# Optimization experiments

Hardware: AMD Instinct MI355X
Metric: run time of the kernel (lower is better)

The kernel has to match this reference:

```python
import jax, jax.numpy as jnp
import numpy as np

GRID_SIZE = 8
MARGIN = 1.0
NUM_NEG = 8
SOS_NEG = 8
LOSS_LAMBDA = 1.0
D_INTER = 4  # d1_inter_num == d2_inter_num == 4 in the source
IMG = 512    # image side in pixels (H * grid_size)


def warp_points(pts, homo):
    ph = jnp.concatenate([pts, jnp.ones_like(pts[..., :1])], axis=-1)  # B,N,3
    q = jnp.einsum('bij,bnj->bni', homo, ph)
    return q[..., :2] / (q[..., 2:3] + 1e-8)


def inv_sim_vec(d1, d2):
    # 2 - 2*<d1,d2> == squared L2 distance for unit-norm descriptors
    return 2.0 - 2.0 * jnp.sum(d1 * d2, axis=-1)


def inv_sim_mat(d1, d2):
    return 2.0 - 2.0 * jnp.einsum('bnc,bmc->bnm', d1, d2)


def sq_dist_mat(p1, p2):
    # squared Euclidean distance; monotone in distance so topk indices and
    # radius comparisons (vs radius**2) match the original exactly.
    n1 = jnp.sum(p1 * p1, axis=-1)
    n2 = jnp.sum(p2 * p2, axis=-1)
    d = n1[:, :, None] + n2[:, None, :] - 2.0 * jnp.einsum('bnd,bmd->bnm', p1, p2)
    return jnp.maximum(d, 0.0)


def topk_smallest(x, k):
    v, i = jax.lax.top_k(-x, k)
    return -v, i


def create_coo_grid(h, w, grid_size):
    ys, xs = jnp.meshgrid(jnp.arange(h, dtype=jnp.float32), jnp.arange(w, dtype=jnp.float32), indexing='ij')
    return jnp.stack([(xs + 0.5) * grid_size, (ys + 0.5) * grid_size], axis=-1).reshape(-1, 2)  # HW,2 (x,y)


def sample_descriptors(desc, kp, grid_size):
    # desc: B,C,H,W; kp: B,N,2 (x,y) image coords. Bilinear sample + L2 normalize.
    b, c, h, w = desc.shape
    x = kp[..., 0] / grid_size - 0.5
    y = kp[..., 1] / grid_size - 0.5
    x0 = jnp.floor(x); y0 = jnp.floor(y)
    wx = x - x0; wy = y - y0
    x0i = jnp.clip(x0.astype(jnp.int32), 0, w - 1); x1i = jnp.clip(x0i + 1, 0, w - 1)
    y0i = jnp.clip(y0.astype(jnp.int32), 0, h - 1); y1i = jnp.clip(y0i + 1, 0, h - 1)
    dflat = desc.transpose(0, 2, 3, 1).reshape(b, h * w, c)  # B,HW,C
    bi = jnp.arange(b)[:, None]
    g = lambda yi, xi: dflat[bi, yi * w + xi]  # B,N,C
    out = ((1 - wx) * (1 - wy))[..., None] * g(y0i, x0i) \
        + (wx * (1 - wy))[..., None] * g(y0i, x1i) \
        + ((1 - wx) * wy)[..., None] * g(y1i, x0i) \
        + (wx * wy)[..., None] * g(y1i, x1i)
    return out / (jnp.linalg.norm(out, axis=-1, keepdims=True) + 1e-8)


def setup_inputs():
    key = jax.random.key(0)
    k1, k2, k3, k4 = jax.random.split(key, 4)
    b, n, c, h, w = 4, 1024, 128, 64, 64
    kp1 = jax.random.uniform(k1, (b, n, 2), dtype=jnp.float32) * (IMG - 1.0)
    kp1_desc = jax.random.normal(k2, (b, n, c), dtype=jnp.float32)
    kp1_desc = kp1_desc / jnp.linalg.norm(kp1_desc, axis=-1, keepdims=True)
    desc2 = jax.random.normal(k3, (b, c, h, w), dtype=jnp.float32)
    homo12 = jnp.broadcast_to(jnp.eye(3, dtype=jnp.float32), (b, 3, 3)) + 0.005 * jax.random.normal(k4, (b, 3, 3), dtype=jnp.float32)
    w_kp1 = jnp.clip(warp_points(kp1, homo12), 0.0, IMG - 1.0)
    return {'kp1': kp1, 'w_kp1': w_kp1, 'kp1_desc': kp1_desc, 'desc2': desc2, 'homo12': homo12}


def reference(kp1, w_kp1, kp1_desc, desc2, homo12):
    b, n, c = kp1_desc.shape
    _, _, h, w = desc2.shape
    hw = h * w
    gs = GRID_SIZE
    bi = jnp.arange(b)[:, None]

    w_kp1_desc = sample_descriptors(desc2, w_kp1, gs)                 # B,N,C
    positive_sim = inv_sim_vec(kp1_desc, w_kp1_desc)                  # B,N

    coo = jnp.broadcast_to(create_coo_grid(h, w, gs), (b, hw, 2))     # B,HW,2
    # 4 nearest grid cells of each kp1, warped into image 2
    _, kp1_cell_ids = topk_smallest(sq_dist_mat(kp1, coo), D_INTER)   # B,N,4
    kp1_cells = coo[bi, kp1_cell_ids.reshape(b, -1)]                  # B,4N,2
    w_kp1_cells = warp_points(kp1_cells, homo12)                      # B,4N,2
    _, kp2_cell_ids = topk_smallest(sq_dist_mat(w_kp1_cells, coo), D_INTER)  # B,4N,4
    mask = jnp.zeros((b, n * D_INTER, hw), dtype=jnp.float32)
    mask = mask.at[jnp.arange(b)[:, None, None], jnp.arange(n * D_INTER)[None, :, None], kp2_cell_ids].set(1.0)
    neigh_mask = mask.reshape(b, n, D_INTER, hw).sum(axis=2)          # B,N,HW

    desc2_flat = desc2.transpose(0, 2, 3, 1).reshape(b, hw, c)
    desc_sim = inv_sim_mat(kp1_desc, desc2_flat) + neigh_mask * 5.0   # B,N,HW
    neg_sim, _ = topk_smallest(desc_sim, NUM_NEG)                     # B,N,num_neg
    fos = jnp.mean(jnp.maximum(positive_sim[:, :, None] - neg_sim + MARGIN, 0.0) ** 2)

    radius2 = (gs * np.sqrt(2.0) + 0.1) ** 2
    kp1_sim = inv_sim_mat(kp1_desc, kp1_desc) + (sq_dist_mat(kp1, kp1) <= radius2).astype(jnp.float32) * 5.0
    w_kp1_sim = inv_sim_mat(w_kp1_desc, w_kp1_desc) + (sq_dist_mat(w_kp1, w_kp1) <= radius2).astype(jnp.float32) * 5.0
    _, kp1_neg_ids = topk_smallest(kp1_sim, SOS_NEG)                  # B,N,sos_neg
    _, w_kp1_neg_ids = topk_smallest(w_kp1_sim, SOS_NEG)
    b3 = jnp.arange(b)[:, None, None]
    kp1_neg_desc = kp1_desc[b3, kp1_neg_ids]                          # B,N,sos_neg,C
    w_kp1_neg_desc = w_kp1_desc[b3, w_kp1_neg_ids]
    sos = inv_sim_vec(kp1_desc[:, :, None, :], kp1_neg_desc) - inv_sim_vec(w_kp1_desc[:, :, None, :], w_kp1_neg_desc)
    sos = jnp.mean(jnp.sqrt(jnp.sum(sos ** 2, axis=-1)))
    return (fos + sos) * LOSS_LAMBDA
```

## Files before the change

kernel.cpp:

```cpp
#include <hip/hip_runtime.h>

#define NB 4
#define NN 1024
#define NCCH 128
#define NH 64
#define NW 64
#define NHW 4096

constexpr float RADIUS2 = 130.27274173013714f;

typedef __attribute__((ext_vector_type(8))) short short8v;
typedef __attribute__((ext_vector_type(4))) float f32x4;

__device__ __forceinline__ unsigned short f2bf(float f) {
    unsigned u = __float_as_uint(f);
    unsigned r = u + 0x7FFFu + ((u >> 16) & 1u);
    return (unsigned short)(r >> 16);
}
__device__ __forceinline__ float bf2f(unsigned short h) {
    return __uint_as_float(((unsigned)h) << 16);
}

__device__ __forceinline__ void bsort8(float* v) {
    #pragma unroll
    for (int d = 4; d >= 1; d >>= 1) {
        #pragma unroll
        for (int i = 0; i < 8; ++i) {
            if ((i & d) == 0) {
                float x = v[i], y = v[i + d];
                v[i] = fminf(x, y);
                v[i + d] = fmaxf(x, y);
            }
        }
    }
}
__device__ __forceinline__ void merge8(const float* a, const float* b, float* o) {
    #pragma unroll
    for (int k = 0; k < 8; ++k) o[k] = fminf(a[k], b[7 - k]);
    bsort8(o);
}

__device__ __forceinline__ void nearest4(float x, float y, int out_ids[4]) {
    float u = x * 0.125f - 0.5f;
    float v = y * 0.125f - 0.5f;
    u = fminf(fmaxf(u, -1e6f), 1e6f);
    v = fminf(fmaxf(v, -1e6f), 1e6f);
    int iu = (int)floorf(u);
    int iv = (int)floorf(v);
    int xlo = min(max(iu - 2, 0), 60);
    int xhi = max(min(iu + 3, 63), 3);
    int ylo = min(max(iv - 2, 0), 60);
    int yhi = max(min(iv + 3, 63), 3);
    float bd0 = 1e30f, bd1 = 1e30f, bd2 = 1e30f, bd3 = 1e30f;
    int bi0 = 0, bi1 = 0, bi2 = 0, bi3 = 0;
    for (int yy = ylo; yy <= yhi; ++yy) {
        float dy = y - ((float)yy + 0.5f) * 8.0f;
        float dy2 = dy * dy;
        for (int xx = xlo; xx <= xhi; ++xx) {
            float dx = x - ((float)xx + 0.5f) * 8.0f;
            float d = dx * dx + dy2;
            int id = (yy << 6) | xx;
            if (d < bd3) {
                if (d < bd2) {
                    bd3 = bd2; bi3 = bi2;
                    if (d < bd1) {
                        bd2 = bd1; bi2 = bi1;
                        if (d < bd0) { bd1 = bd0; bi1 = bi0; bd0 = d; bi0 = id; }
                        else         { bd1 = d;  bi1 = id; }
                    } else { bd2 = d; bi2 = id; }
                } else { bd3 = d; bi3 = id; }
            }
        }
    }
    out_ids[0] = bi0; out_ids[1] = bi1; out_ids[2] = bi2; out_ids[3] = bi3;
}

__global__ __launch_bounds__(256) void d2split_kernel(
    const float* __restrict__ desc2,
    unsigned short* __restrict__ d2hi, unsigned short* __restrict__ d2lo,
    float* __restrict__ d2T, int use_t)
{
    __shared__ float sT[64][33];
    int bid = blockIdx.x;
    int b = bid >> 8;
    int rem = bid & 255;
    int hw0 = (rem >> 2) * 64;
    int c0 = (rem & 3) * 32;
    int t = threadIdx.x;

    {
        int lane = t & 63, cg = t >> 6;
        const float* src = desc2 + (size_t)b * NCCH * NHW + hw0 + lane;
        #pragma unroll
        for (int i = 0; i < 8; ++i) {
            int cl = cg * 8 + i;
            sT[lane][cl] = src[(size_t)(c0 + cl) * NHW];
        }
    }
    __syncthreads();
    {
        int hw = t >> 2, q = t & 3;
        size_t base = ((size_t)b * NHW + hw0 + hw) * NCCH + c0 + q * 8;
        unsigned short hb[8], lb[8];
        float fb[8];
        #pragma unroll
        for (int i = 0; i < 8; ++i) {
            float f = sT[hw][q * 8 + i];
            unsigned short h = f2bf(f);
            hb[i] = h;
            lb[i] = f2bf(f - bf2f(h));
            fb[i] = f;
        }
        *(short8v*)(d2hi + base) = *(short8v*)hb;
        *(short8v*)(d2lo + base) = *(short8v*)lb;
        if (use_t) {
            *(float4*)(d2T + base) = *(float4*)&fb[0];
            *(float4*)(d2T + base + 4) = *(float4*)&fb[4];
        }
    }
}

__global__ __launch_bounds__(256) void sample_mask_kernel(
    const float* __restrict__ kp1, const float* __restrict__ w_kp1,
    const float* __restrict__ kp1_desc, const float* __restrict__ desc2,
    const float* __restrict__ d2T, int use_t,
    const float* __restrict__ homo,
    unsigned short* __restrict__ khi, unsigned short* __restrict__ klo,
    unsigned short* __restrict__ whi, unsigned short* __restrict__ wlo,
    float* __restrict__ pos_sim, int* __restrict__ mask_ids)
{
    int bid = blockIdx.x;
    if (bid >= 1024) {
        int g = (bid - 1024) * 256 + threadIdx.x;
        if (g >= NB * NN) return;
        int b = g >> 10;
        float x = kp1[g * 2], y = kp1[g * 2 + 1];
        const float* H = homo + b * 9;
        int c4[4];
        nearest4(x, y, c4);
        int out[16];
        #pragma unroll
        for (int k = 0; k < 4; ++k) {
            int id = c4[k];
            float cx = ((float)(id & 63) + 0.5f) * 8.0f;
            float cy = ((float)(id >> 6) + 0.5f) * 8.0f;
            float q0 = H[0] * cx + H[1] * cy + H[2];
            float q1 = H[3] * cx + H[4] * cy + H[5];
            float q2 = H[6] * cx + H[7] * cy + H[8];
            float iz = 1.0f / (q2 + 1e-8f);
            nearest4(q0 * iz, q1 * iz, out + 4 * k);
        }
        #pragma unroll
        for (int k = 0; k < 16; ++k) mask_ids[(size_t)g * 16 + k] = out[k];
        return;
    }

    int lane = threadIdx.x & 63;
    int wid = bid * 4 + (threadIdx.x >> 6);
    int b = wid >> 10;

    float px = w_kp1[wid * 2 + 0], py = w_kp1[wid * 2 + 1];
    float fx = px * 0.125f - 0.5f, fy = py * 0.125f - 0.5f;
    float fx0 = floorf(fx), fy0 = floorf(fy);
    float wx = fx - fx0, wy = fy - fy0;
    int x0 = min(max((int)fx0, 0), NW - 1);
    int x1 = min(x0 + 1, NW - 1);
    int y0 = min(max((int)fy0, 0), NH - 1);
    int y1 = min(y0 + 1, NH - 1);
    float w00 = (1.f - wx) * (1.f - wy), w01 = wx * (1.f - wy);
    float w10 = (1.f - wx) * wy,         w11 = wx * wy;
    int i00 = y0 * NW + x0, i01 = y0 * NW + x1;
    int i10 = y1 * NW + x0, i11 = y1 * NW + x1;

    float o0, o1;
    if (use_t) {
        const float* base = d2T + (size_t)b * NHW * NCCH;
        const float* r00 = base + (size_t)i00 * NCCH;
        const float* r01 = base + (size_t)i01 * NCCH;
        const float* r10 = base + (size_t)i10 * NCCH;
        const float* r11 = base + (size_t)i11 * NCCH;
        o0 = w00 * r00[lane] + w01 * r01[lane] + w10 * r10[lane] + w11 * r11[lane];
        o1 = w00 * r00[lane + 64] + w01 * r01[lane + 64]
           + w10 * r10[lane + 64] + w11 * r11[lane + 64];
    } else {
        const float* d2 = desc2 + (size_t)b * NCCH * NHW;
        const float* p0 = d2 + (size_t)lane * NHW;
        const float* p1 = d2 + (size_t)(lane + 64) * NHW;
        o0 = w00 * p0[i00] + w01 * p0[i01] + w10 * p0[i10] + w11 * p0[i11];
        o1 = w00 * p1[i00] + w01 * p1[i01] + w10 * p1[i10] + w11 * p1[i11];
    }
    float nrm = o0 * o0 + o1 * o1;
    #pragma unroll
    for (int off = 32; off > 0; off >>= 1) nrm += __shfl_xor(nrm, off, 64);
    float inv = 1.0f / (sqrtf(nrm) + 1e-8f);
    o0 *= inv; o1 *= inv;

    float a0 = kp1_desc[(size_t)wid * NCCH + lane];
    float a1 = kp1_desc[(size_t)wid * NCCH + lane + 64];
    float dot = a0 * o0 + a1 * o1;
    #pragma unroll
    for (int off = 32; off > 0; off >>= 1) dot += __shfl_xor(dot, off, 64);

    size_t base = (size_t)wid * NCCH;
    unsigned short h;
    h = f2bf(a0); khi[base + lane] = h;      klo[base + lane] = f2bf(a0 - bf2f(h));
    h = f2bf(a1); khi[base + lane + 64] = h; klo[base + lane + 64] = f2bf(a1 - bf2f(h));
    h = f2bf(o0); whi[base + lane] = h;      wlo[base + lane] = f2bf(o0 - bf2f(h));
    h = f2bf(o1); whi[base + lane + 64] = h; wlo[base + lane + 64] = f2bf(o1 - bf2f(h));
    if (lane == 0) pos_sim[wid] = 2.0f - 2.0f * dot;
}

__global__ __launch_bounds__(256, 4) void simtop_fused(
    const unsigned short* __restrict__ khi, const unsigned short* __restrict__ klo,
    const unsigned short* __restrict__ whi, const unsigned short* __restrict__ wlo,
    const unsigned short* __restrict__ d2hi, const unsigned short* __restrict__ d2lo,
    const float* __restrict__ kp1, const float* __restrict__ w_kp1,
    const int* __restrict__ mask_ids,
    float* __restrict__ fosP, float* __restrict__ sosAP, float* __restrict__ sosBP)
{
    __shared__ float sChunk[32][257];
    __shared__ int   sMask[32][16];
    __shared__ float sCx[256], sCy[256];
    __shared__ float sRx[32], sRy[32];

    int tid = threadIdx.x;
    int bid = blockIdx.x;

    int mode, cs, rg, b, nchunk, colbase, outStride;
    const unsigned short *AH, *AL, *BH, *BL;
    const float* coords = nullptr;
    float* outP;
    if (bid < 512) {
        mode = 0; b = bid >> 7; int rem = bid & 127;
        cs = rem & 3; rg = rem >> 2;
        nchunk = 4; colbase = cs * 1024;
        AH = khi + (size_t)b * NN * NCCH;  AL = klo + (size_t)b * NN * NCCH;
        BH = d2hi + (size_t)b * NHW * NCCH; BL = d2lo + (size_t)b * NHW * NCCH;
        outP = fosP; outStride = 32;
    } else if (bid < 768) {
        int id = bid - 512;
        mode = 1; b = id >> 6; int rem = id & 63;
        cs = rem & 1; rg = rem >> 1;
        nchunk = 2; colbase = cs * 512;
        AH = khi + (size_t)b * NN * NCCH;  AL = klo + (size_t)b * NN * NCCH;
        BH = AH; BL = AL;
        coords = kp1; outP = sosAP; outStride = 16;
    } else {
        int id = bid - 768;
        mode = 2; b = id >> 6; int rem = id & 63;
        cs = rem & 1; rg = rem >> 1;
        nchunk = 2; colbase = cs * 512;
        AH = whi + (size_t)b * NN * NCCH;  AL = wlo + (size_t)b * NN * NCCH;
        BH = AH; BL = AL;
        coords = w_kp1; outP = sosBP; outStride = 16;
    }
    int row0 = rg * 32;

    int lane = tid & 63, wg = tid >> 6;
    int lrow = lane & 15, lgrp = lane >> 4;
    int srow = tid & 31, sgrp = tid >> 5;

    short8v ahi[2][4], alo[2][4];
    #pragma unroll
    for (int rt = 0; rt < 2; ++rt) {
        const unsigned short* aH = AH + (size_t)(row0 + rt * 16 + lrow) * NCCH + lgrp * 8;
        const unsigned short* aL = AL + (size_t)(row0 + rt * 16 + lrow) * NCCH + lgrp * 8;
        #pragma unroll
        for (int s = 0; s < 4; ++s) {
            ahi[rt][s] = *(const short8v*)(aH + s * 32);
            alo[rt][s] = *(const short8v*)(aL + s * 32);
        }
    }

    if (mode == 0) {
        for (int e = tid; e < 512; e += 256)
            sMask[e >> 4][e & 15] =
                mask_ids[((size_t)b * NN + row0 + (e >> 4)) * 16 + (e & 15)];
    } else if (tid < 32) {
        sRx[tid] = coords[((size_t)b * NN + row0 + tid) * 2];
        sRy[tid] = coords[((size_t)b * NN + row0 + tid) * 2 + 1];
    }

    float loc[8];
    #pragma unroll
    for (int k = 0; k < 8; ++k) loc[k] = 1e30f;

    for (int ch = 0; ch < nchunk; ++ch) {
        int cglob = colbase + ch * 256;
        __syncthreads();

        int colq = cglob + wg * 64;
        #pragma unroll
        for (int np = 0; np < 2; ++np) {
            const unsigned short* b0H = BH + (size_t)(colq + (np * 2 + 0) * 16 + lrow) * NCCH + lgrp * 8;
            const unsigned short* b0L = BL + (size_t)(colq + (np * 2 + 0) * 16 + lrow) * NCCH + lgrp * 8;
            const unsigned short* b1H = BH + (size_t)(colq + (np * 2 + 1) * 16 + lrow) * NCCH + lgrp * 8;
            const unsigned short* b1L = BL + (size_t)(colq + (np * 2 + 1) * 16 + lrow) * NCCH + lgrp * 8;
            f32x4 a00 = {0.f, 0.f, 0.f, 0.f}, a01 = {0.f, 0.f, 0.f, 0.f};
            f32x4 a10 = {0.f, 0.f, 0.f, 0.f}, a11 = {0.f, 0.f, 0.f, 0.f};
            #pragma unroll
            for (int s = 0; s < 4; ++s) {
                short8v bh0 = *(const short8v*)(b0H + s * 32);
                short8v bl0 = *(const short8v*)(b0L + s * 32);
                short8v bh1 = *(const short8v*)(b1H + s * 32);
                short8v bl1 = *(const short8v*)(b1L + s * 32);
                a00 = __builtin_amdgcn_mfma_f32_16x16x32_bf16(ahi[0][s], bh0, a00, 0, 0, 0);
                a10 = __builtin_amdgcn_mfma_f32_16x16x32_bf16(ahi[1][s], bh0, a10, 0, 0, 0);
                a01 = __builtin_amdgcn_mfma_f32_16x16x32_bf16(ahi[0][s], bh1, a01, 0, 0, 0);
                a11 = __builtin_amdgcn_mfma_f32_16x16x32_bf16(ahi[1][s], bh1, a11, 0, 0, 0);
                a00 = __builtin_amdgcn_mfma_f32_16x16x32_bf16(ahi[0][s], bl0, a00, 0, 0, 0);
                a10 = __builtin_amdgcn_mfma_f32_16x16x32_bf16(ahi[1][s], bl0, a10, 0, 0, 0);
                a01 = __builtin_amdgcn_mfma_f32_16x16x32_bf16(ahi[0][s], bl1, a01, 0, 0, 0);
                a11 = __builtin_amdgcn_mfma_f32_16x16x32_bf16(ahi[1][s], bl1, a11, 0, 0, 0);
                a00 = __builtin_amdgcn_mfma_f32_16x16x32_bf16(alo[0][s], bh0, a00, 0, 0, 0);
                a10 = __builtin_amdgcn_mfma_f32_16x16x32_bf16(alo[1][s], bh0, a10, 0, 0, 0);
                a01 = __builtin_amdgcn_mfma_f32_16x16x32_bf16(alo[0][s], bh1, a01, 0, 0, 0);
                a11 = __builtin_amdgcn_mfma_f32_16x16x32_bf16(alo[1][s], bh1, a11, 0, 0, 0);
            }
            #pragma unroll
            for (int r = 0; r < 4; ++r) {
                sChunk[lgrp * 4 + r][wg * 64 + (np * 2 + 0) * 16 + lrow]      = 2.0f - 2.0f * a00[r];
                sChunk[16 + lgrp * 4 + r][wg * 64 + (np * 2 + 0) * 16 + lrow] = 2.0f - 2.0f * a10[r];
                sChunk[lgrp * 4 + r][wg * 64 + (np * 2 + 1) * 16 + lrow]      = 2.0f - 2.0f * a01[r];
                sChunk[16 + lgrp * 4 + r][wg * 64 + (np * 2 + 1) * 16 + lrow] = 2.0f - 2.0f * a11[r];
            }
        }
        __syncthreads();

        if (mode == 0) {
            for (int e = tid; e < 512; e += 256) {
                int r = e >> 4;
                int id = sMask[r][e & 15] - cglob;
                if (id >= 0 && id < 256) atomicAdd(&sChunk[r][id], 5.0f);
            }
        } else {
            sCx[tid] = coords[((size_t)b * NN + cglob + tid) * 2];
            sCy[tid] = coords[((size_t)b * NN + cglob + tid) * 2 + 1];
        }
        __syncthreads();

        float rx = 0.f, ry = 0.f;
        if (mode != 0) { rx = sRx[srow]; ry = sRy[srow]; }
        #pragma unroll
        for (int j = 0; j < 32; ++j) {
            int cl = sgrp * 32 + j;
            float v = sChunk[srow][cl];
            if (mode != 0) {
                float dx = rx - sCx[cl], dy = ry - sCy[cl];
                if (dx * dx + dy * dy <= RADIUS2) v += 5.0f;
            }
            if (v < loc[7]) {
                loc[7] = v;
                #pragma unroll
                for (int p = 7; p > 0; --p) {
                    if (loc[p - 1] > loc[p]) {
                        float t = loc[p - 1]; loc[p - 1] = loc[p]; loc[p] = t;
                    }
                }
            }
        }
    }

    __syncthreads();
    float* mg = &sChunk[0][0];
    #pragma unroll
    for (int k = 0; k < 8; ++k) mg[srow * 67 + sgrp * 8 + k] = loc[k];
    __syncthreads();
    #pragma unroll
    for (int step = 1; step < 8; step <<= 1) {
        if ((sgrp & (2 * step - 1)) == 0) {
            float a[8], bb[8], o[8];
            #pragma unroll
            for (int k = 0; k < 8; ++k) {
                a[k]  = mg[srow * 67 + sgrp * 8 + k];
                bb[k] = mg[srow * 67 + (sgrp + step) * 8 + k];
            }
            merge8(a, bb, o);
            #pragma unroll
            for (int k = 0; k < 8; ++k) mg[srow * 67 + sgrp * 8 + k] = o[k];
        }
        __syncthreads();
    }
    if (tid < 32) {
        size_t row = (size_t)b * NN + row0 + tid;
        #pragma unroll
        for (int k = 0; k < 8; ++k)
            outP[row * outStride + cs * 8 + k] = mg[tid * 67 + k];
    }
}

__global__ __launch_bounds__(256) void frow_kernel(
    const float* __restrict__ fosP, const float* __restrict__ sosAP,
    const float* __restrict__ sosBP, const float* __restrict__ pos_sim,
    float* __restrict__ frow, float* __restrict__ srow)
{
    int row = blockIdx.x * 256 + threadIdx.x;
    if (row >= NB * NN) return;

    float l0[8], l1[8], l2[8], l3[8], t0[8], t1[8], m[8];
    const float4* fp = (const float4*)(fosP + (size_t)row * 32);
    float4 q;
    q = fp[0]; l0[0]=q.x; l0[1]=q.y; l0[2]=q.z; l0[3]=q.w;
    q = fp[1]; l0[4]=q.x; l0[5]=q.y; l0[6]=q.z; l0[7]=q.w;
    q = fp[2]; l1[0]=q.x; l1[1]=q.y; l1[2]=q.z; l1[3]=q.w;
    q = fp[3]; l1[4]=q.x; l1[5]=q.y; l1[6]=q.z; l1[7]=q.w;
    q = fp[4]; l2[0]=q.x; l2[1]=q.y; l2[2]=q.z; l2[3]=q.w;
    q = fp[5]; l2[4]=q.x; l2[5]=q.y; l2[6]=q.z; l2[7]=q.w;
    q = fp[6]; l3[0]=q.x; l3[1]=q.y; l3[2]=q.z; l3[3]=q.w;
    q = fp[7]; l3[4]=q.x; l3[5]=q.y; l3[6]=q.z; l3[7]=q.w;
    merge8(l0, l1, t0); merge8(l2, l3, t1); merge8(t0, t1, m);

    float p = pos_sim[row], fs = 0.f;
    #pragma unroll
    for (int k = 0; k < 8; ++k) {
        float h = fmaxf(p - m[k] + 1.0f, 0.f);
        fs += h * h;
    }

    const float4* ap = (const float4*)(sosAP + (size_t)row * 16);
    q = ap[0]; l0[0]=q.x; l0[1]=q.y; l0[2]=q.z; l0[3]=q.w;
    q = ap[1]; l0[4]=q.x; l0[5]=q.y; l0[6]=q.z; l0[7]=q.w;
    q = ap[2]; l1[0]=q.x; l1[1]=q.y; l1[2]=q.z; l1[3]=q.w;
    q = ap[3]; l1[4]=q.x; l1[5]=q.y; l1[6]=q.z; l1[7]=q.w;
    merge8(l0, l1, t0);
    const float4* bp = (const float4*)(sosBP + (size_t)row * 16);
    q = bp[0]; l2[0]=q.x; l2[1]=q.y; l2[2]=q.z; l2[3]=q.w;
    q = bp[1]; l2[4]=q.x; l2[5]=q.y; l2[6]=q.z; l2[7]=q.w;
    q = bp[2]; l3[0]=q.x; l3[1]=q.y; l3[2]=q.z; l3[3]=q.w;
    q = bp[3]; l3[4]=q.x; l3[5]=q.y; l3[6]=q.z; l3[7]=q.w;
    merge8(l2, l3, t1);

    float acc = 0.f;
    #pragma unroll
    for (int k = 0; k < 8; ++k) {
        float d = t0[k] - t1[k];
        acc += d * d;
    }
    frow[row] = fs;
    srow[row] = sqrtf(acc);
}

__global__ __launch_bounds__(256) void freduce_kernel(
    const float* __restrict__ frow, const float* __restrict__ srow,
    float* __restrict__ outp)
{
    __shared__ float sf[256], ss[256];
    int t = threadIdx.x;
    float f = 0.f, s = 0.f;
    for (int i = t; i < NB * NN; i += 256) { f += frow[i]; s += srow[i]; }
    sf[t] = f; ss[t] = s;
    __syncthreads();
    for (int o = 128; o > 0; o >>= 1) {
        if (t < o) { sf[t] += sf[t + o]; ss[t] += ss[t + o]; }
        __syncthreads();
    }
    if (t == 0)
        outp[0] = sf[0] / (float)(NB * NN * 8) + ss[0] / (float)(NB * NN);
}

extern "C" void kernel_launch(void* const* d_in, const int* in_sizes, int n_in,
                              void* d_out, int out_size, void* d_ws, size_t ws_size,
                              hipStream_t stream) {
    const float* kp1      = (const float*)d_in[0];
    const float* w_kp1    = (const float*)d_in[1];
    const float* kp1_desc = (const float*)d_in[2];
    const float* desc2    = (const float*)d_in[3];
    const float* homo     = (const float*)d_in[4];
    float* outp = (float*)d_out;

    char* ws = (char*)d_ws;
    size_t o = 0;
    unsigned short* khi  = (unsigned short*)(ws + o); o += (size_t)NB * NN * NCCH * 2;
    unsigned short* klo  = (unsigned short*)(ws + o); o += (size_t)NB * NN * NCCH * 2;
    unsigned short* whi  = (unsigned short*)(ws + o); o += (size_t)NB * NN * NCCH * 2;
    unsigned short* wlo  = (unsigned short*)(ws + o); o += (size_t)NB * NN * NCCH * 2;
    unsigned short* d2hi = (unsigned short*)(ws + o); o += (size_t)NB * NHW * NCCH * 2;
    unsigned short* d2lo = (unsigned short*)(ws + o); o += (size_t)NB * NHW * NCCH * 2;
    float* pos_sim = (float*)(ws + o); o += (size_t)NB * NN * 4;
    float* fosP    = (float*)(ws + o); o += (size_t)NB * NN * 32 * 4;
    float* sosAP   = (float*)(ws + o); o += (size_t)NB * NN * 16 * 4;
    float* sosBP   = (float*)(ws + o); o += (size_t)NB * NN * 16 * 4;
    float* frow    = (float*)(ws + o); o += (size_t)NB * NN * 4;
    float* srow    = (float*)(ws + o); o += (size_t)NB * NN * 4;
    int*   mask_id = (int*)(ws + o);   o += (size_t)NB * NN * 16 * 4;
    float* d2T     = (float*)(ws + o);
    size_t need_t  = o + (size_t)NB * NHW * NCCH * 4;
    int use_t = (ws_size >= need_t) ? 1 : 0;
    if (!use_t) d2T = (float*)ws;

    d2split_kernel<<<NB * 256, 256, 0, stream>>>(desc2, d2hi, d2lo, d2T, use_t);
    sample_mask_kernel<<<1040, 256, 0, stream>>>(kp1, w_kp1, kp1_desc, desc2,
                                                 d2T, use_t, homo,
                                                 khi, klo, whi, wlo,
                                                 pos_sim, mask_id);
    simtop_fused<<<1024, 256, 0, stream>>>(khi, klo, whi, wlo, d2hi, d2lo,
                                           kp1, w_kp1, mask_id,
                                           fosP, sosAP, sosBP);
    frow_kernel<<<16, 256, 0, stream>>>(fosP, sosAP, sosBP, pos_sim, frow, srow);
    freduce_kernel<<<1, 256, 0, stream>>>(frow, srow, outp);
}
```

Measured before the change: 199.7 us.

## Halve column chunk size and remap blocks so each XCD shares operand panels

The column chunk processed per iteration shrinks from 256 to 128, which halves the shared-memory tile and the per-wave MFMA tile, so more chunks run per block. Block indices are also reassigned so that blocks on the same XCD (bid mod 8) work on the same batch and column slice, improving L2 reuse of the B operand across that XCD's blocks. The trade-off is less MFMA work per synchronisation, more barriers per block, and a launch grid that must still total 1024 blocks in the new layout.

```diff
diff --git a/kernel.cpp b/kernel.cpp
--- a/kernel.cpp
+++ b/kernel.cpp
@@ -6,6 +6,7 @@
 #define NH 64
 #define NW 64
 #define NHW 4096
+#define CHUNK 128
 
 constexpr float RADIUS2 = 130.27274173013714f;
 
@@ -218,38 +219,36 @@
     const int* __restrict__ mask_ids,
     float* __restrict__ fosP, float* __restrict__ sosAP, float* __restrict__ sosBP)
 {
-    __shared__ float sChunk[32][257];
+    __shared__ float sChunk[32][CHUNK + 1];
     __shared__ int   sMask[32][16];
-    __shared__ float sCx[256], sCy[256];
+    __shared__ float sCx[CHUNK], sCy[CHUNK];
     __shared__ float sRx[32], sRy[32];
 
     int tid = threadIdx.x;
     int bid = blockIdx.x;
-
-    int mode, cs, rg, b, nchunk, colbase, outStride;
+    int xcd = bid & 7, slot = bid >> 3;
+    int gl = slot >> 5, rg = slot & 31;
+
+    int mode, cs, b, nchunk, colbase, outStride;
     const unsigned short *AH, *AL, *BH, *BL;
     const float* coords = nullptr;
     float* outP;
-    if (bid < 512) {
-        mode = 0; b = bid >> 7; int rem = bid & 127;
-        cs = rem & 3; rg = rem >> 2;
-        nchunk = 4; colbase = cs * 1024;
+    if (gl < 2) {
+        int g = xcd + 8 * gl;
+        mode = 0; b = g >> 2; cs = g & 3;
+        nchunk = 8; colbase = cs * 1024;
         AH = khi + (size_t)b * NN * NCCH;  AL = klo + (size_t)b * NN * NCCH;
         BH = d2hi + (size_t)b * NHW * NCCH; BL = d2lo + (size_t)b * NHW * NCCH;
         outP = fosP; outStride = 32;
-    } else if (bid < 768) {
-        int id = bid - 512;
-        mode = 1; b = id >> 6; int rem = id & 63;
-        cs = rem & 1; rg = rem >> 1;
-        nchunk = 2; colbase = cs * 512;
+    } else if (gl == 2) {
+        mode = 1; b = xcd >> 1; cs = xcd & 1;
+        nchunk = 4; colbase = cs * 512;
         AH = khi + (size_t)b * NN * NCCH;  AL = klo + (size_t)b * NN * NCCH;
         BH = AH; BL = AL;
         coords = kp1; outP = sosAP; outStride = 16;
     } else {
-        int id = bid - 768;
-        mode = 2; b = id >> 6; int rem = id & 63;
-        cs = rem & 1; rg = rem >> 1;
-        nchunk = 2; colbase = cs * 512;
+        mode = 2; b = xcd >> 1; cs = xcd & 1;
+        nchunk = 4; colbase = cs * 512;
         AH = whi + (size_t)b * NN * NCCH;  AL = wlo + (size_t)b * NN * NCCH;
         BH = AH; BL = AL;
         coords = w_kp1; outP = sosBP; outStride = 16;
@@ -286,16 +285,15 @@
     for (int k = 0; k < 8; ++k) loc[k] = 1e30f;
 
     for (int ch = 0; ch < nchunk; ++ch) {
-        int cglob = colbase + ch * 256;
+        int cglob = colbase + ch * CHUNK;
         __syncthreads();
 
-        int colq = cglob + wg * 64;
-        #pragma unroll
-        for (int np = 0; np < 2; ++np) {
-            const unsigned short* b0H = BH + (size_t)(colq + (np * 2 + 0) * 16 + lrow) * NCCH + lgrp * 8;
-            const unsigned short* b0L = BL + (size_t)(colq + (np * 2 + 0) * 16 + lrow) * NCCH + lgrp * 8;
-            const unsigned short* b1H = BH + (size_t)(colq + (np * 2 + 1) * 16 + lrow) * NCCH + lgrp * 8;
-            const unsigned short* b1L = BL + (size_t)(colq + (np * 2 + 1) * 16 + lrow) * NCCH + lgrp * 8;
+        int colq = cglob + wg * 32;
+        {
+            const unsigned short* b0H = BH + (size_t)(colq + lrow) * NCCH + lgrp * 8;
+            const unsigned short* b0L = BL + (size_t)(colq + lrow) * NCCH + lgrp * 8;
+            const unsigned short* b1H = BH + (size_t)(colq + 16 + lrow) * NCCH + lgrp * 8;
+            const unsigned short* b1L = BL + (size_t)(colq + 16 + lrow) * NCCH + lgrp * 8;
             f32x4 a00 = {0.f, 0.f, 0.f, 0.f}, a01 = {0.f, 0.f, 0.f, 0.f};
             f32x4 a10 = {0.f, 0.f, 0.f, 0.f}, a11 = {0.f, 0.f, 0.f, 0.f};
             #pragma unroll
@@ -319,10 +317,10 @@
             }
             #pragma unroll
             for (int r = 0; r < 4; ++r) {
-                sChunk[lgrp * 4 + r][wg * 64 + (np * 2 + 0) * 16 + lrow]      = 2.0f - 2.0f * a00[r];
-                sChunk[16 + lgrp * 4 + r][wg * 64 + (np * 2 + 0) * 16 + lrow] = 2.0f - 2.0f * a10[r];
-                sChunk[lgrp * 4 + r][wg * 64 + (np * 2 + 1) * 16 + lrow]      = 2.0f - 2.0f * a01[r];
-                sChunk[16 + lgrp * 4 + r][wg * 64 + (np * 2 + 1) * 16 + lrow] = 2.0f - 2.0f * a11[r];
+                sChunk[lgrp * 4 + r][wg * 32 + lrow]           = 2.0f - 2.0f * a00[r];
+                sChunk[16 + lgrp * 4 + r][wg * 32 + lrow]      = 2.0f - 2.0f * a10[r];
+                sChunk[lgrp * 4 + r][wg * 32 + 16 + lrow]      = 2.0f - 2.0f * a01[r];
+                sChunk[16 + lgrp * 4 + r][wg * 32 + 16 + lrow] = 2.0f - 2.0f * a11[r];
             }
         }
         __syncthreads();
@@ -331,19 +329,21 @@
             for (int e = tid; e < 512; e += 256) {
                 int r = e >> 4;
                 int id = sMask[r][e & 15] - cglob;
-                if (id >= 0 && id < 256) atomicAdd(&sChunk[r][id], 5.0f);
+                if (id >= 0 && id < CHUNK) atomicAdd(&sChunk[r][id], 5.0f);
             }
         } else {
-            sCx[tid] = coords[((size_t)b * NN + cglob + tid) * 2];
-            sCy[tid] = coords[((size_t)b * NN + cglob + tid) * 2 + 1];
+            if (tid < CHUNK)
+                sCx[tid] = coords[((size_t)b * NN + cglob + tid) * 2];
+            else
+                sCy[tid - CHUNK] = coords[((size_t)b * NN + cglob + (tid - CHUNK)) * 2 + 1];
         }
         __syncthreads();
 
         float rx = 0.f, ry = 0.f;
         if (mode != 0) { rx = sRx[srow]; ry = sRy[srow]; }
         #pragma unroll
-        for (int j = 0; j < 32; ++j) {
-            int cl = sgrp * 32 + j;
+        for (int j = 0; j < 16; ++j) {
+            int cl = sgrp * 16 + j;
             float v = sChunk[srow][cl];
             if (mode != 0) {
                 float dx = rx - sCx[cl], dy = ry - sCy[cl];
```

Result: faster. 177.2 us (-11.3%).
